# Kernel tuning notes

Measured on AMD Instinct MI355X. Metric: run time of the kernel, lower is better.

Reference implementation:

```python
import jax, jax.numpy as jnp
import numpy as np

B, H, S = 64, 1024, 512
MIN_VAL, MAX_VAL = -1.0, 1.0
EPS = 1e-8  # torch F.cosine_similarity default eps


def setup_inputs() -> dict:
    key = jax.random.key(0)
    k1, k2, k3 = jax.random.split(key, 3)
    tree_state = jax.random.normal(k1, (B, H), dtype=jnp.float32)
    seq_states = jax.random.normal(k2, (B, H, S), dtype=jnp.float32)
    # binary validity mask (float, as it is multiplied in)
    seq_mask = (jax.random.uniform(k3, (B, S)) < 0.9).astype(jnp.float32)
    return {"tree_state": tree_state, "seq_states": seq_states, "seq_mask": seq_mask}


def reference(tree_state, seq_states, seq_mask):
    # scan over the seq axis; carry h: (B, H)
    xs = (jnp.transpose(seq_states, (2, 0, 1)), seq_mask.T)  # (S,B,H), (S,B)

    def step(h, x):
        s, m = x  # s: (B,H), m: (B,)
        dot = jnp.sum(h * s, axis=-1)  # (B,)
        denom = jnp.maximum(
            jnp.linalg.norm(h, axis=-1) * jnp.linalg.norm(s, axis=-1), EPS
        )
        cos = (dot / denom)[:, None]  # (B,1)
        h_new = jnp.clip(h + (s - h * cos) * m[:, None], MIN_VAL, MAX_VAL)
        return h_new, None

    h, _ = jax.lax.scan(step, tree_state, xs)
    return h
```

## Files before the change

### kernel.cpp

```cpp
#include <hip/hip_runtime.h>


#define NB 64
#define NH 1024
#define NS 512

typedef float v4f __attribute__((ext_vector_type(4)));

template <int N> struct ic { static constexpr int value = N; };

template <int CTRL>
__device__ __forceinline__ float dpp_add(float x) {
  int s = __builtin_amdgcn_update_dpp(0, __builtin_bit_cast(int, x), CTRL, 0xf,
                                      0xf, true);
  return x + __builtin_bit_cast(float, s);
}

__device__ __forceinline__ void wave_red3_to63(float& a, float& b, float& c) {
  a = dpp_add<0x111>(a); b = dpp_add<0x111>(b); c = dpp_add<0x111>(c);
  a = dpp_add<0x112>(a); b = dpp_add<0x112>(b); c = dpp_add<0x112>(c);
  a = dpp_add<0x114>(a); b = dpp_add<0x114>(b); c = dpp_add<0x114>(c);
  a = dpp_add<0x118>(a); b = dpp_add<0x118>(b); c = dpp_add<0x118>(c);
  a = dpp_add<0x142>(a); b = dpp_add<0x142>(b); c = dpp_add<0x142>(c);
  a = dpp_add<0x143>(a); b = dpp_add<0x143>(b); c = dpp_add<0x143>(c);
}

#define GLD4(dst, p) \
  asm volatile("global_load_dwordx4 %0, %1, off" : "=v"(dst) : "v"(p))
#define GLD1(dst, p) \
  asm volatile("global_load_dword %0, %1, off" : "=v"(dst) : "v"(p))

template <int IMM>
__device__ __forceinline__ void dsr128(v4f& d, unsigned a) {
  asm volatile("ds_read_b128 %[d], %[a] offset:%[o]"
               : [d] "=v"(d)
               : [a] "v"(a), [o] "n"(IMM));
}
template <int IMM>
__device__ __forceinline__ void dsw32(unsigned a, float v) {
  asm volatile("ds_write_b32 %[a], %[v] offset:%[o]" ::[a] "v"(a), [v] "v"(v),
               [o] "n"(IMM));
}

#define VMW3(r) asm volatile("s_waitcnt vmcnt(3)" : "+v"(r))
#define LGK0SV(sv) asm volatile("s_waitcnt lgkmcnt(0)" : "+v"(sv))
#define LGK5PR(p0, p1, p2)                  \
  asm volatile("s_waitcnt lgkmcnt(5)"       \
               : "+v"(p0), "+v"(p1), "+v"(p2))

template <int S>
__device__ __forceinline__ void stage_write(unsigned wb, v4f rg) {
  dsw32<0 * 4096 + 64 * S>(wb, rg[0]);
  dsw32<1 * 4096 + 64 * S>(wb, rg[1]);
  dsw32<2 * 4096 + 64 * S>(wb, rg[2]);
  dsw32<3 * 4096 + 64 * S>(wb, rg[3]);
}

__global__ __launch_bounds__(256, 1) void otsu_scan_kernel(
    const float* __restrict__ tree,
    const float* __restrict__ seq,
    const float* __restrict__ mask,
    float* __restrict__ out) {
  __shared__ float lds[2 * 16 * 1024 + 64];
  const int b = blockIdx.x;
  const int tid = threadIdx.x;
  const int w = tid >> 6;
  const int l = tid & 63;

  const float* hrow = tree + b * NH + 256 * w + 4 * l;
  v4f h;
  GLD4(h, hrow);
  float m8[8];
  {
    const float* mp = mask + b * NS + l;
    GLD1(m8[0], mp);
    GLD1(m8[1], mp + 64);
    GLD1(m8[2], mp + 128);
    GLD1(m8[3], mp + 192);
    GLD1(m8[4], mp + 256);
    GLD1(m8[5], mp + 320);
    GLD1(m8[6], mp + 384);
    GLD1(m8[7], mp + 448);
  }
  asm volatile("s_waitcnt vmcnt(0)"
               : "+v"(h), "+v"(m8[0]), "+v"(m8[1]), "+v"(m8[2]), "+v"(m8[3]),
                 "+v"(m8[4]), "+v"(m8[5]), "+v"(m8[6]), "+v"(m8[7]));

  unsigned mbits = 0u;
#pragma unroll
  for (int i = 0; i < 8; ++i)
    if (m8[i] != 0.0f) mbits |= (1u << i);

  if (!(__builtin_amdgcn_readlane((int)mbits, 0) & 1)) {
#pragma unroll
    for (int i = 0; i < 4; ++i)
      h[i] = __builtin_amdgcn_fmed3f(h[i], -1.0f, 1.0f);
  }

  const float* sp0 = seq + (size_t)b * NH * NS + (size_t)w * 131072 +
                     (l >> 2) * 512 + (l & 3) * 4;
  const float* sp = sp0;
  const unsigned lb = (unsigned)(unsigned long long)(&lds[0]);
  unsigned rb = lb + 1024u * (unsigned)w + 16u * (unsigned)l;
  unsigned wbase =
      lb + 16384u * (unsigned)(l & 3) + 1024u * (unsigned)w +
      4u * (unsigned)(l >> 2);
  const unsigned vp = lb + 131072u + 4u * (unsigned)w;
  const unsigned pb = lb + 131072u;

  v4f ring[8];
  v4f sval[2];

  GLD4(ring[0], sp); sp += 8192;
  GLD4(ring[1], sp); sp += 8192;
  GLD4(ring[2], sp); sp += 8192;
  GLD4(ring[3], sp); sp += 8192;
#define PCH(c)                                              \
  do {                                                      \
    VMW3(ring[(c) & 7]);                                    \
    stage_write<(c)>(wbase, ring[(c) & 7]);                 \
    if ((c) == 12) sp -= 131056;     \
    GLD4(ring[((c) + 4) & 7], sp);                          \
    sp += 8192;                                             \
  } while (0)
  PCH(0);  PCH(1);  PCH(2);  PCH(3);
  PCH(4);  PCH(5);  PCH(6);  PCH(7);
  PCH(8);  PCH(9);  PCH(10); PCH(11);
  PCH(12); PCH(13); PCH(14); PCH(15);
#undef PCH

  dsr128<0>(sval[0], rb);

  unsigned wb = wbase ^ 0x10000u;

#pragma unroll 1
  for (int g = 0; g < 32; ++g) {
    const int lbase = (16 * g) & 63;
    const int msh = g >> 2;
    auto step = [&](auto sc) {
      constexpr int S = decltype(sc)::value;
      LGK0SV(sval[S & 1]);
      const unsigned mw =
          (unsigned)__builtin_amdgcn_readlane((int)mbits, lbase + S);
      const bool act = (mw >> msh) & 1u;
      v4f pr0, pr1, pr2;
      if (act) {
        const v4f s = sval[S & 1];
        float pd0 = h[0] * s[0]; pd0 = fmaf(h[1], s[1], pd0);
        float pd1 = h[2] * s[2]; pd1 = fmaf(h[3], s[3], pd1);
        float ph0 = h[0] * h[0]; ph0 = fmaf(h[1], h[1], ph0);
        float ph1 = h[2] * h[2]; ph1 = fmaf(h[3], h[3], ph1);
        float ps0 = s[0] * s[0]; ps0 = fmaf(s[1], s[1], ps0);
        float ps1 = s[2] * s[2]; ps1 = fmaf(s[3], s[3], ps1);
        float pd = pd0 + pd1, ph = ph0 + ph1, ps = ps0 + ps1;
        wave_red3_to63(pd, ph, ps);
        if (l == 63) {
          dsw32<(S & 3) * 64 + 0>(vp, pd);
          dsw32<(S & 3) * 64 + 16>(vp, ph);
          dsw32<(S & 3) * 64 + 32>(vp, ps);
        }
        asm volatile("s_waitcnt lgkmcnt(0)" ::: "memory");
      }
      asm volatile("s_barrier" ::: "memory");
      if (act) {
        dsr128<(S & 3) * 64 + 0>(pr0, pb);
        dsr128<(S & 3) * 64 + 16>(pr1, pb);
        dsr128<(S & 3) * 64 + 32>(pr2, pb);
      }
      VMW3(ring[S & 7]);
      stage_write<S>(wb, ring[S & 7]);
      if constexpr (S == 12) sp = (g < 30) ? sp - 131056 : sp0;
      GLD4(ring[(S + 4) & 7], sp);
      sp += 8192;
      if constexpr (S < 15) dsr128<(S + 1) * 4096>(sval[(S + 1) & 1], rb);
      else                  dsr128<0>(sval[0], rb ^ 0x10000u);
      if (act) {
        LGK5PR(pr0, pr1, pr2);
        float dot = (pr0[0] + pr0[1]) + (pr0[2] + pr0[3]);
        float hh = (pr1[0] + pr1[1]) + (pr1[2] + pr1[3]);
        float ss = (pr2[0] + pr2[1]) + (pr2[2] + pr2[3]);
        const float p = fmaxf(hh * ss, 1e-16f);
        const float c = dot * __builtin_amdgcn_rsqf(p);
        const float a = 1.0f - c;
        const v4f s = sval[S & 1];
#pragma unroll
        for (int i = 0; i < 4; ++i)
          h[i] = __builtin_amdgcn_fmed3f(fmaf(h[i], a, s[i]), -1.0f, 1.0f);
      }
    };
    step(ic<0>{});  step(ic<1>{});  step(ic<2>{});  step(ic<3>{});
    step(ic<4>{});  step(ic<5>{});  step(ic<6>{});  step(ic<7>{});
    step(ic<8>{});  step(ic<9>{});  step(ic<10>{}); step(ic<11>{});
    step(ic<12>{}); step(ic<13>{}); step(ic<14>{}); step(ic<15>{});
    rb ^= 0x10000u;
    wb ^= 0x10000u;
  }

  asm volatile("s_waitcnt vmcnt(0) lgkmcnt(0)" ::: "memory");

  float* orow = out + b * NH + 256 * w + 4 * l;
  float4 v;
  v.x = h[0];
  v.y = h[1];
  v.z = h[2];
  v.w = h[3];
  *(float4*)orow = v;
}

extern "C" void kernel_launch(void* const* d_in, const int* in_sizes, int n_in,
                              void* d_out, int out_size, void* d_ws,
                              size_t ws_size, hipStream_t stream) {
  const float* tree = (const float*)d_in[0];
  const float* seq = (const float*)d_in[1];
  const float* mask = (const float*)d_in[2];
  float* out = (float*)d_out;
  otsu_scan_kernel<<<dim3(NB), dim3(256), 0, stream>>>(tree, seq, mask, out);
}
```

Measured before the change: 310.7 us.

## Specialize warps: one compute wave owns full row, three waves stage loads

The scan is restructured so wave 0 holds the entire 1024-wide h vector (16 floats per lane) and performs each step's reduction entirely within the wave, using DPP plus readlane. This removes the per-step cross-wave LDS exchange and block barrier. Waves 1-3 act as producers, loading 16-step chunks of the sequence from global memory into a double-buffered LDS region, with only one barrier per 16 steps. Packed FP32 math (v_pk_fma/mul/add) cuts the compute instruction count. The trade-off is that the serial compute now runs on a single wave with four times the work per step, and producers issue bulk loads followed by a full vmcnt wait instead of a streaming ring.

```diff
diff --git a/kernel.cpp b/kernel.cpp
--- a/kernel.cpp
+++ b/kernel.cpp
@@ -6,6 +6,7 @@
 #define NS 512
 
 typedef float v4f __attribute__((ext_vector_type(4)));
+typedef float v2f __attribute__((ext_vector_type(2)));
 
 template <int N> struct ic { static constexpr int value = N; };
 
@@ -16,13 +17,21 @@
   return x + __builtin_bit_cast(float, s);
 }
 
-__device__ __forceinline__ void wave_red3_to63(float& a, float& b, float& c) {
+__device__ __forceinline__ float readlane_f(float v, int lane) {
+  return __builtin_bit_cast(
+      float, __builtin_amdgcn_readlane(__builtin_bit_cast(int, v), lane));
+}
+
+__device__ __forceinline__ void wave_red3(float& a, float& b, float& c) {
   a = dpp_add<0x111>(a); b = dpp_add<0x111>(b); c = dpp_add<0x111>(c);
   a = dpp_add<0x112>(a); b = dpp_add<0x112>(b); c = dpp_add<0x112>(c);
   a = dpp_add<0x114>(a); b = dpp_add<0x114>(b); c = dpp_add<0x114>(c);
   a = dpp_add<0x118>(a); b = dpp_add<0x118>(b); c = dpp_add<0x118>(c);
   a = dpp_add<0x142>(a); b = dpp_add<0x142>(b); c = dpp_add<0x142>(c);
   a = dpp_add<0x143>(a); b = dpp_add<0x143>(b); c = dpp_add<0x143>(c);
+  a = readlane_f(a, 63);
+  b = readlane_f(b, 63);
+  c = readlane_f(c, 63);
 }
 
 #define GLD4(dst, p) \
@@ -42,169 +51,209 @@
                [o] "n"(IMM));
 }
 
-#define VMW3(r) asm volatile("s_waitcnt vmcnt(3)" : "+v"(r))
-#define LGK0SV(sv) asm volatile("s_waitcnt lgkmcnt(0)" : "+v"(sv))
-#define LGK5PR(p0, p1, p2)                  \
-  asm volatile("s_waitcnt lgkmcnt(5)"       \
-               : "+v"(p0), "+v"(p1), "+v"(p2))
-
-template <int S>
-__device__ __forceinline__ void stage_write(unsigned wb, v4f rg) {
-  dsw32<0 * 4096 + 64 * S>(wb, rg[0]);
-  dsw32<1 * 4096 + 64 * S>(wb, rg[1]);
-  dsw32<2 * 4096 + 64 * S>(wb, rg[2]);
-  dsw32<3 * 4096 + 64 * S>(wb, rg[3]);
-}
+__device__ __forceinline__ v2f pk_fma(v2f a, v2f b, v2f c) {
+  v2f d;
+  asm("v_pk_fma_f32 %0, %1, %2, %3" : "=v"(d) : "v"(a), "v"(b), "v"(c));
+  return d;
+}
+__device__ __forceinline__ v2f pk_mul(v2f a, v2f b) {
+  v2f d;
+  asm("v_pk_mul_f32 %0, %1, %2" : "=v"(d) : "v"(a), "v"(b));
+  return d;
+}
+__device__ __forceinline__ v2f pk_add(v2f a, v2f b) {
+  v2f d;
+  asm("v_pk_add_f32 %0, %1, %2" : "=v"(d) : "v"(a), "v"(b));
+  return d;
+}
+
+#define LGK0SV(s0, s1, s2, s3)                                       \
+  asm volatile("s_waitcnt lgkmcnt(0)"                                \
+               : "+v"(s0), "+v"(s1), "+v"(s2), "+v"(s3))
 
 __global__ __launch_bounds__(256, 1) void otsu_scan_kernel(
     const float* __restrict__ tree,
     const float* __restrict__ seq,
     const float* __restrict__ mask,
     float* __restrict__ out) {
-  __shared__ float lds[2 * 16 * 1024 + 64];
+  __shared__ float lds[2 * 16 * 1024];
   const int b = blockIdx.x;
   const int tid = threadIdx.x;
   const int w = tid >> 6;
   const int l = tid & 63;
-
-  const float* hrow = tree + b * NH + 256 * w + 4 * l;
-  v4f h;
-  GLD4(h, hrow);
-  float m8[8];
-  {
-    const float* mp = mask + b * NS + l;
-    GLD1(m8[0], mp);
-    GLD1(m8[1], mp + 64);
-    GLD1(m8[2], mp + 128);
-    GLD1(m8[3], mp + 192);
-    GLD1(m8[4], mp + 256);
-    GLD1(m8[5], mp + 320);
-    GLD1(m8[6], mp + 384);
-    GLD1(m8[7], mp + 448);
-  }
-  asm volatile("s_waitcnt vmcnt(0)"
-               : "+v"(h), "+v"(m8[0]), "+v"(m8[1]), "+v"(m8[2]), "+v"(m8[3]),
-                 "+v"(m8[4]), "+v"(m8[5]), "+v"(m8[6]), "+v"(m8[7]));
-
-  unsigned mbits = 0u;
-#pragma unroll
-  for (int i = 0; i < 8; ++i)
-    if (m8[i] != 0.0f) mbits |= (1u << i);
-
-  if (!(__builtin_amdgcn_readlane((int)mbits, 0) & 1)) {
-#pragma unroll
-    for (int i = 0; i < 4; ++i)
-      h[i] = __builtin_amdgcn_fmed3f(h[i], -1.0f, 1.0f);
-  }
-
-  const float* sp0 = seq + (size_t)b * NH * NS + (size_t)w * 131072 +
-                     (l >> 2) * 512 + (l & 3) * 4;
-  const float* sp = sp0;
   const unsigned lb = (unsigned)(unsigned long long)(&lds[0]);
-  unsigned rb = lb + 1024u * (unsigned)w + 16u * (unsigned)l;
-  unsigned wbase =
-      lb + 16384u * (unsigned)(l & 3) + 1024u * (unsigned)w +
-      4u * (unsigned)(l >> 2);
-  const unsigned vp = lb + 131072u + 4u * (unsigned)w;
-  const unsigned pb = lb + 131072u;
-
-  v4f ring[8];
-  v4f sval[2];
-
-  GLD4(ring[0], sp); sp += 8192;
-  GLD4(ring[1], sp); sp += 8192;
-  GLD4(ring[2], sp); sp += 8192;
-  GLD4(ring[3], sp); sp += 8192;
-#define PCH(c)                                              \
-  do {                                                      \
-    VMW3(ring[(c) & 7]);                                    \
-    stage_write<(c)>(wbase, ring[(c) & 7]);                 \
-    if ((c) == 12) sp -= 131056;     \
-    GLD4(ring[((c) + 4) & 7], sp);                          \
-    sp += 8192;                                             \
-  } while (0)
-  PCH(0);  PCH(1);  PCH(2);  PCH(3);
-  PCH(4);  PCH(5);  PCH(6);  PCH(7);
-  PCH(8);  PCH(9);  PCH(10); PCH(11);
-  PCH(12); PCH(13); PCH(14); PCH(15);
-#undef PCH
-
-  dsr128<0>(sval[0], rb);
-
-  unsigned wb = wbase ^ 0x10000u;
+
+  if (w == 0) {
+    const float* hrow = tree + b * NH + 4 * l;
+    v4f hv0, hv1, hv2, hv3;
+    GLD4(hv0, hrow);
+    asm volatile("global_load_dwordx4 %0, %1, off offset:1024"
+                 : "=v"(hv1) : "v"(hrow));
+    asm volatile("global_load_dwordx4 %0, %1, off offset:2048"
+                 : "=v"(hv2) : "v"(hrow));
+    asm volatile("global_load_dwordx4 %0, %1, off offset:3072"
+                 : "=v"(hv3) : "v"(hrow));
+    float m8[8];
+    {
+      const float* mp = mask + b * NS + l;
+      GLD1(m8[0], mp);
+      GLD1(m8[1], mp + 64);
+      GLD1(m8[2], mp + 128);
+      GLD1(m8[3], mp + 192);
+      GLD1(m8[4], mp + 256);
+      GLD1(m8[5], mp + 320);
+      GLD1(m8[6], mp + 384);
+      GLD1(m8[7], mp + 448);
+    }
+    asm volatile("s_waitcnt vmcnt(0)"
+                 : "+v"(hv0), "+v"(hv1), "+v"(hv2), "+v"(hv3), "+v"(m8[0]),
+                   "+v"(m8[1]), "+v"(m8[2]), "+v"(m8[3]), "+v"(m8[4]),
+                   "+v"(m8[5]), "+v"(m8[6]), "+v"(m8[7]));
+
+    v2f h2[8];
+    h2[0] = v2f{hv0[0], hv0[1]}; h2[1] = v2f{hv0[2], hv0[3]};
+    h2[2] = v2f{hv1[0], hv1[1]}; h2[3] = v2f{hv1[2], hv1[3]};
+    h2[4] = v2f{hv2[0], hv2[1]}; h2[5] = v2f{hv2[2], hv2[3]};
+    h2[6] = v2f{hv3[0], hv3[1]}; h2[7] = v2f{hv3[2], hv3[3]};
+
+    unsigned mbits = 0u;
+#pragma unroll
+    for (int i = 0; i < 8; ++i)
+      if (m8[i] != 0.0f) mbits |= (1u << i);
+
+    if (!(__builtin_amdgcn_readlane((int)mbits, 0) & 1)) {
+#pragma unroll
+      for (int p = 0; p < 8; ++p) {
+        h2[p].x = __builtin_amdgcn_fmed3f(h2[p].x, -1.0f, 1.0f);
+        h2[p].y = __builtin_amdgcn_fmed3f(h2[p].y, -1.0f, 1.0f);
+      }
+    }
+
+    unsigned rb = lb + 16u * (unsigned)l;
+    v4f sval[2][4];
+
+    asm volatile("s_barrier" ::: "memory");
 
 #pragma unroll 1
-  for (int g = 0; g < 32; ++g) {
-    const int lbase = (16 * g) & 63;
-    const int msh = g >> 2;
-    auto step = [&](auto sc) {
-      constexpr int S = decltype(sc)::value;
-      LGK0SV(sval[S & 1]);
-      const unsigned mw =
-          (unsigned)__builtin_amdgcn_readlane((int)mbits, lbase + S);
-      const bool act = (mw >> msh) & 1u;
-      v4f pr0, pr1, pr2;
-      if (act) {
-        const v4f s = sval[S & 1];
-        float pd0 = h[0] * s[0]; pd0 = fmaf(h[1], s[1], pd0);
-        float pd1 = h[2] * s[2]; pd1 = fmaf(h[3], s[3], pd1);
-        float ph0 = h[0] * h[0]; ph0 = fmaf(h[1], h[1], ph0);
-        float ph1 = h[2] * h[2]; ph1 = fmaf(h[3], h[3], ph1);
-        float ps0 = s[0] * s[0]; ps0 = fmaf(s[1], s[1], ps0);
-        float ps1 = s[2] * s[2]; ps1 = fmaf(s[3], s[3], ps1);
-        float pd = pd0 + pd1, ph = ph0 + ph1, ps = ps0 + ps1;
-        wave_red3_to63(pd, ph, ps);
-        if (l == 63) {
-          dsw32<(S & 3) * 64 + 0>(vp, pd);
-          dsw32<(S & 3) * 64 + 16>(vp, ph);
-          dsw32<(S & 3) * 64 + 32>(vp, ps);
+    for (int g = 0; g < 32; ++g) {
+      const int lbase = (16 * g) & 63;
+      const int msh = g >> 2;
+      dsr128<0 * 4096 + 0>(sval[0][0], rb);
+      dsr128<0 * 4096 + 1024>(sval[0][1], rb);
+      dsr128<0 * 4096 + 2048>(sval[0][2], rb);
+      dsr128<0 * 4096 + 3072>(sval[0][3], rb);
+      auto step = [&](auto sc) {
+        constexpr int T = decltype(sc)::value;
+        LGK0SV(sval[T & 1][0], sval[T & 1][1], sval[T & 1][2],
+               sval[T & 1][3]);
+        if constexpr (T < 15) {
+          dsr128<(T + 1) * 4096 + 0>(sval[(T + 1) & 1][0], rb);
+          dsr128<(T + 1) * 4096 + 1024>(sval[(T + 1) & 1][1], rb);
+          dsr128<(T + 1) * 4096 + 2048>(sval[(T + 1) & 1][2], rb);
+          dsr128<(T + 1) * 4096 + 3072>(sval[(T + 1) & 1][3], rb);
         }
-        asm volatile("s_waitcnt lgkmcnt(0)" ::: "memory");
+        const unsigned mw =
+            (unsigned)__builtin_amdgcn_readlane((int)mbits, lbase + T);
+        if ((mw >> msh) & 1u) {
+          const v4f s0 = sval[T & 1][0], s1 = sval[T & 1][1],
+                    s2 = sval[T & 1][2], s3 = sval[T & 1][3];
+          v2f sp[8];
+          sp[0] = v2f{s0[0], s0[1]}; sp[1] = v2f{s0[2], s0[3]};
+          sp[2] = v2f{s1[0], s1[1]}; sp[3] = v2f{s1[2], s1[3]};
+          sp[4] = v2f{s2[0], s2[1]}; sp[5] = v2f{s2[2], s2[3]};
+          sp[6] = v2f{s3[0], s3[1]}; sp[7] = v2f{s3[2], s3[3]};
+          v2f a0 = pk_mul(h2[0], sp[0]), a1 = pk_mul(h2[1], sp[1]);
+          v2f a2 = pk_mul(h2[2], sp[2]), a3 = pk_mul(h2[3], sp[3]);
+          v2f b0 = pk_mul(h2[0], h2[0]), b1 = pk_mul(h2[1], h2[1]);
+          v2f b2 = pk_mul(h2[2], h2[2]), b3 = pk_mul(h2[3], h2[3]);
+          v2f c0 = pk_mul(sp[0], sp[0]), c1 = pk_mul(sp[1], sp[1]);
+          v2f c2 = pk_mul(sp[2], sp[2]), c3 = pk_mul(sp[3], sp[3]);
+          a0 = pk_fma(h2[4], sp[4], a0); a1 = pk_fma(h2[5], sp[5], a1);
+          a2 = pk_fma(h2[6], sp[6], a2); a3 = pk_fma(h2[7], sp[7], a3);
+          b0 = pk_fma(h2[4], h2[4], b0); b1 = pk_fma(h2[5], h2[5], b1);
+          b2 = pk_fma(h2[6], h2[6], b2); b3 = pk_fma(h2[7], h2[7], b3);
+          c0 = pk_fma(sp[4], sp[4], c0); c1 = pk_fma(sp[5], sp[5], c1);
+          c2 = pk_fma(sp[6], sp[6], c2); c3 = pk_fma(sp[7], sp[7], c3);
+          v2f A = pk_add(pk_add(a0, a1), pk_add(a2, a3));
+          v2f Bv = pk_add(pk_add(b0, b1), pk_add(b2, b3));
+          v2f C = pk_add(pk_add(c0, c1), pk_add(c2, c3));
+          float pd = A.x + A.y, ph = Bv.x + Bv.y, ps = C.x + C.y;
+          wave_red3(pd, ph, ps);
+          const float p = fmaxf(ph * ps, 1e-16f);
+          const float cc = pd * __builtin_amdgcn_rsqf(p);
+          const float aa = 1.0f - cc;
+          const v2f av = v2f{aa, aa};
+#pragma unroll
+          for (int q = 0; q < 8; ++q) {
+            v2f t = pk_fma(h2[q], av, sp[q]);
+            h2[q].x = __builtin_amdgcn_fmed3f(t.x, -1.0f, 1.0f);
+            h2[q].y = __builtin_amdgcn_fmed3f(t.y, -1.0f, 1.0f);
+          }
+        }
+      };
+      step(ic<0>{});  step(ic<1>{});  step(ic<2>{});  step(ic<3>{});
+      step(ic<4>{});  step(ic<5>{});  step(ic<6>{});  step(ic<7>{});
+      step(ic<8>{});  step(ic<9>{});  step(ic<10>{}); step(ic<11>{});
+      step(ic<12>{}); step(ic<13>{}); step(ic<14>{}); step(ic<15>{});
+      rb ^= 0x10000u;
+      asm volatile("s_barrier" ::: "memory");
+    }
+
+    asm volatile("s_waitcnt vmcnt(0) lgkmcnt(0)" ::: "memory");
+    float* orow = out + b * NH + 4 * l;
+#pragma unroll
+    for (int m = 0; m < 4; ++m) {
+      float4 v;
+      v.x = h2[2 * m].x;
+      v.y = h2[2 * m].y;
+      v.z = h2[2 * m + 1].x;
+      v.w = h2[2 * m + 1].y;
+      *(float4*)(orow + 256 * m) = v;
+    }
+  } else {
+    const float* pbase = seq + (size_t)b * NH * NS + (l >> 2) * 512 +
+                         (l & 3) * 4;
+    const unsigned wpb =
+        lb + 16384u * (unsigned)(l & 3) + 4u * (unsigned)(l >> 2);
+    const int cb = w - 1;
+
+    v4f ring[22];
+#define STAGE(T_, BSEL_)                                                  \
+    do {                                                                  \
+      _Pragma("unroll") for (int k = 0; k < 22; ++k) {                    \
+        const int c = 3 * k + cb;                                         \
+        if (c < 64) {                                                     \
+          const float* p_ = pbase + c * 8192 + (T_) * 16;                 \
+          GLD4(ring[k], p_);                                              \
+        }                                                                 \
+      }                                                                   \
+      asm volatile("s_waitcnt vmcnt(0)" ::: "memory");                    \
+      _Pragma("unroll") for (int k = 0; k < 22; ++k) {                    \
+        const int c = 3 * k + cb;                                         \
+        if (c < 64) {                                                     \
+          const unsigned a_ = wpb + (BSEL_) + 64u * (unsigned)c;          \
+          dsw32<0>(a_, ring[k][0]);                                       \
+          dsw32<4096>(a_, ring[k][1]);                                    \
+          dsw32<8192>(a_, ring[k][2]);                                    \
+          dsw32<12288>(a_, ring[k][3]);                                   \
+        }                                                                 \
+      }                                                                   \
+      asm volatile("s_waitcnt lgkmcnt(0)" ::: "memory");                  \
+    } while (0)
+
+    STAGE(0, 0u);
+    asm volatile("s_barrier" ::: "memory");
+
+#pragma unroll 1
+    for (int g = 0; g < 32; ++g) {
+      if (g < 31) {
+        const unsigned bsel = (unsigned)((g + 1) & 1) << 16;
+        STAGE(g + 1, bsel);
       }
       asm volatile("s_barrier" ::: "memory");
-      if (act) {
-        dsr128<(S & 3) * 64 + 0>(pr0, pb);
-        dsr128<(S & 3) * 64 + 16>(pr1, pb);
-        dsr128<(S & 3) * 64 + 32>(pr2, pb);
-      }
-      VMW3(ring[S & 7]);
-      stage_write<S>(wb, ring[S & 7]);
-      if constexpr (S == 12) sp = (g < 30) ? sp - 131056 : sp0;
-      GLD4(ring[(S + 4) & 7], sp);
-      sp += 8192;
-      if constexpr (S < 15) dsr128<(S + 1) * 4096>(sval[(S + 1) & 1], rb);
-      else                  dsr128<0>(sval[0], rb ^ 0x10000u);
-      if (act) {
-        LGK5PR(pr0, pr1, pr2);
-        float dot = (pr0[0] + pr0[1]) + (pr0[2] + pr0[3]);
-        float hh = (pr1[0] + pr1[1]) + (pr1[2] + pr1[3]);
-        float ss = (pr2[0] + pr2[1]) + (pr2[2] + pr2[3]);
-        const float p = fmaxf(hh * ss, 1e-16f);
-        const float c = dot * __builtin_amdgcn_rsqf(p);
-        const float a = 1.0f - c;
-        const v4f s = sval[S & 1];
-#pragma unroll
-        for (int i = 0; i < 4; ++i)
-          h[i] = __builtin_amdgcn_fmed3f(fmaf(h[i], a, s[i]), -1.0f, 1.0f);
-      }
-    };
-    step(ic<0>{});  step(ic<1>{});  step(ic<2>{});  step(ic<3>{});
-    step(ic<4>{});  step(ic<5>{});  step(ic<6>{});  step(ic<7>{});
-    step(ic<8>{});  step(ic<9>{});  step(ic<10>{}); step(ic<11>{});
-    step(ic<12>{}); step(ic<13>{}); step(ic<14>{}); step(ic<15>{});
-    rb ^= 0x10000u;
-    wb ^= 0x10000u;
+    }
+#undef STAGE
   }
-
-  asm volatile("s_waitcnt vmcnt(0) lgkmcnt(0)" ::: "memory");
-
-  float* orow = out + b * NH + 256 * w + 4 * l;
-  float4 v;
-  v.x = h[0];
-  v.y = h[1];
-  v.z = h[2];
-  v.w = h[3];
-  *(float4*)orow = v;
 }
 
 extern "C" void kernel_launch(void* const* d_in, const int* in_sizes, int n_in,
```

New measurement: 270.4 us. 1.15x faster.
